# Performance work log

Hardware: AMD Instinct MI355X
Metric: run time of the kernel (lower is better)

The kernel has to match this reference:

```python
import jax, jax.numpy as jnp
import numpy as np

N, E, H, R = 16384, 262144, 256, 64
INV_SQRT_3 = 1.0 / np.sqrt(3.0)
INV_SQRT_H = 1.0 / np.sqrt(float(H))
INV_SQRT_2 = 1.0 / np.sqrt(2.0)


def ssilu(t):
    # ScaledSiLU: silu(x) / 0.6
    return jax.nn.silu(t) * (1.0 / 0.6)


def layernorm(x, g, b):
    m = jnp.mean(x, axis=-1, keepdims=True)
    v = jnp.var(x, axis=-1, keepdims=True)
    return (x - m) * jax.lax.rsqrt(v + 1e-5) * g + b


def gated_equivariant_block(x, v, Wv1, Wv2, Wu1, bu1, Wu2, bu2, out_ch):
    # x: [N, Cin], v: [N, 3, Cin]
    vec1 = jnp.linalg.norm(v @ Wv1, axis=-2)          # [N, Cin]
    vec2 = v @ Wv2                                     # [N, 3, out_ch]
    h = ssilu(jnp.concatenate([x, vec1], axis=-1) @ Wu1 + bu1) @ Wu2 + bu2
    xn, vn = h[..., :out_ch], h[..., out_ch:]
    return ssilu(xn), vn[:, None, :] * vec2


def setup_inputs() -> dict:
    key = jax.random.key(0)
    ks = iter(jax.random.split(key, 48))

    def w(shape, fan_in):
        return jax.random.normal(next(ks), shape, jnp.float32) / np.sqrt(float(fan_in))

    return {
        "x": jax.random.normal(next(ks), (N, H), jnp.float32),
        "vec": jax.random.normal(next(ks), (N, 3, H), jnp.float32),
        "edge_rbf": jax.random.uniform(next(ks), (E, R), jnp.float32),
        "edge_vector": jax.random.normal(next(ks), (E, 3), jnp.float32),
        # PaiNNMessage params
        "ln_g": jnp.ones((H,), jnp.float32), "ln_b": jnp.zeros((H,), jnp.float32),
        "W_x1": w((H, H), H), "b_x1": jnp.zeros((H,), jnp.float32),
        "W_x2": w((H, 3 * H), H), "b_x2": jnp.zeros((3 * H,), jnp.float32),
        "W_rbf": w((R, 3 * H), R), "b_rbf": jnp.zeros((3 * H,), jnp.float32),
        # PaiNNUpdate params
        "W_vp": w((H, 2 * H), H),
        "W_xv1": w((2 * H, H), 2 * H), "b_xv1": jnp.zeros((H,), jnp.float32),
        "W_xv2": w((H, 3 * H), H), "b_xv2": jnp.zeros((3 * H,), jnp.float32),
        # PaiNNOutput block 1 (H -> H//2)
        "o1_Wv1": w((H, H), H), "o1_Wv2": w((H, H // 2), H),
        "o1_Wu1": w((2 * H, H), 2 * H), "o1_bu1": jnp.zeros((H,), jnp.float32),
        "o1_Wu2": w((H, H), H), "o1_bu2": jnp.zeros((H,), jnp.float32),
        # PaiNNOutput block 2 (H//2 -> 1)
        "o2_Wv1": w((H // 2, H // 2), H // 2), "o2_Wv2": w((H // 2, 1), H // 2),
        "o2_Wu1": w((H, H // 2), H), "o2_bu1": jnp.zeros((H // 2,), jnp.float32),
        "o2_Wu2": w((H // 2, 2), H // 2), "o2_bu2": jnp.zeros((2,), jnp.float32),
        "edge_index": jax.random.randint(next(ks), (2, E), 0, N),
    }


def reference(x, vec, edge_rbf, edge_vector,
              ln_g, ln_b, W_x1, b_x1, W_x2, b_x2, W_rbf, b_rbf,
              W_vp, W_xv1, b_xv1, W_xv2, b_xv2,
              o1_Wv1, o1_Wv2, o1_Wu1, o1_bu1, o1_Wu2, o1_bu2,
              o2_Wv1, o2_Wv2, o2_Wu1, o2_bu1, o2_Wu2, o2_bu2,
              edge_index):
    src, dst = edge_index[0], edge_index[1]

    # ---- PaiNNMessage ----
    xh = ssilu(layernorm(x, ln_g, ln_b) @ W_x1 + b_x1) @ W_x2 + b_x2   # [N, 3H]
    rbfh = edge_rbf @ W_rbf + b_rbf                                     # [E, 3H]
    m = xh[src] * rbfh                                                  # gather + fuse
    m1, m2, m3 = m[:, :H], m[:, H:2 * H], m[:, 2 * H:]
    m2 = m2 * INV_SQRT_3
    vmsg = (vec[src] * m2[:, None, :] + m3[:, None, :] * edge_vector[:, :, None]) * INV_SQRT_H  # [E,3,H]
    dx = jax.ops.segment_sum(m1, dst, num_segments=N)
    dvec = jax.ops.segment_sum(vmsg, dst, num_segments=N)
    x = x + dx
    vec = vec + dvec

    # ---- PaiNNUpdate ----
    vp = vec @ W_vp                                    # [N, 3, 2H]
    vec1, vec2 = vp[..., :H], vp[..., H:]
    vec_dot = jnp.sum(vec1 * vec2, axis=1) * INV_SQRT_H            # [N, H]
    vnorm = jnp.sqrt(jnp.sum(vec2 * vec2, axis=-2) + 1e-8)          # [N, H]
    xvh = ssilu(jnp.concatenate([x, vnorm], axis=-1) @ W_xv1 + b_xv1) @ W_xv2 + b_xv2
    xv1, xv2, xv3 = xvh[:, :H], xvh[:, H:2 * H], xvh[:, 2 * H:]
    x = x + (xv1 + xv2 * vec_dot) * INV_SQRT_2
    vec = vec + xv3[:, None, :] * vec1

    # ---- PaiNNOutput ----
    x, vec = gated_equivariant_block(x, vec, o1_Wv1, o1_Wv2, o1_Wu1, o1_bu1, o1_Wu2, o1_bu2, H // 2)
    x, vec = gated_equivariant_block(x, vec, o2_Wv1, o2_Wv2, o2_Wu1, o2_bu1, o2_Wu2, o2_bu2, 1)
    return jnp.squeeze(vec, axis=-1)   # [N, 3]
```

## Files before the change

kernel.cpp:

```cpp
#include <hip/hip_runtime.h>
#include <math.h>

#define NN 16384
#define EE 262144
#define HH 256

#define INV_SQRT_3f 0.57735026918962576f
#define INV_SQRT_Hf 0.0625f
#define INV_SQRT_2f 0.70710678118654752f
#define SSILU_SCALE 1.6666666666666667f

typedef __attribute__((ext_vector_type(8))) short bf16x8;
typedef __attribute__((ext_vector_type(4))) float f32x4;

__device__ __forceinline__ float ssilu_f(float v) {
    return v * (1.0f / (1.0f + __expf(-v))) * SSILU_SCALE;
}
__device__ __forceinline__ float b2f(short s) {
    unsigned int u = ((unsigned int)(unsigned short)s) << 16;
    return __uint_as_float(u);
}
__device__ __forceinline__ short f2b(float f) {
    unsigned int u = __float_as_uint(f);
    unsigned int r = (u + 0x7fff + ((u >> 16) & 1)) >> 16;
    return (short)r;
}

__global__ void __launch_bounds__(256) ln_kernel(const float* __restrict__ x,
                                                 const float* __restrict__ g,
                                                 const float* __restrict__ b,
                                                 short* __restrict__ oh,
                                                 short* __restrict__ ol) {
    int n = blockIdx.x;
    int t = threadIdx.x;
    float v = x[(long)n * HH + t];
    float s = v, s2 = v * v;
    #pragma unroll
    for (int off = 32; off > 0; off >>= 1) {
        s  += __shfl_down(s, off);
        s2 += __shfl_down(s2, off);
    }
    __shared__ float red[8];
    int wave = t >> 6, lane = t & 63;
    if (lane == 0) { red[wave] = s; red[4 + wave] = s2; }
    __syncthreads();
    __shared__ float mr[2];
    if (t == 0) {
        float ts = red[0] + red[1] + red[2] + red[3];
        float ts2 = red[4] + red[5] + red[6] + red[7];
        float mean = ts * (1.0f / HH);
        float var = ts2 * (1.0f / HH) - mean * mean;
        mr[0] = mean;
        mr[1] = rsqrtf(var + 1e-5f);
    }
    __syncthreads();
    float o = (v - mr[0]) * mr[1] * g[t] + b[t];
    short hh = f2b(o);
    oh[(long)n * HH + t] = hh;
    ol[(long)n * HH + t] = f2b(o - b2f(hh));
}

struct WtArgs {
    const float* W[11];
    int K[11];
    int N[11];
    int off[12];
};

__global__ void __launch_bounds__(256) wt_split_all(WtArgs a,
                                                    short* __restrict__ WTh,
                                                    short* __restrict__ WTl) {
    int idx = blockIdx.x * 256 + threadIdx.x;
    int s = 0;
    #pragma unroll
    for (int i = 1; i < 11; i++) s += (idx >= a.off[i]) ? 1 : 0;
    int local = idx - a.off[s];
    int K = a.K[s], N = a.N[s];
    int k = local / N, n = local - k * N;
    float w = a.W[s][local];
    short hh = f2b(w);
    long o = (long)a.off[s] + (long)n * K + k;
    WTh[o] = hh;
    WTl[o] = f2b(w - b2f(hh));
}

__global__ void __launch_bounds__(256) split4_kernel(const float* __restrict__ in,
                                                     short* __restrict__ h,
                                                     short* __restrict__ l) {
    long i = ((long)blockIdx.x * 256 + threadIdx.x) * 4;
    float4 v = *(const float4*)(in + i);
    short4 oh, ol;
    oh.x = f2b(v.x); ol.x = f2b(v.x - b2f(oh.x));
    oh.y = f2b(v.y); ol.y = f2b(v.y - b2f(oh.y));
    oh.z = f2b(v.z); ol.z = f2b(v.z - b2f(oh.z));
    oh.w = f2b(v.w); ol.w = f2b(v.w - b2f(oh.w));
    *(short4*)(h + i) = oh;
    *(short4*)(l + i) = ol;
}

__global__ void __launch_bounds__(256) mfma_gemm(const short* __restrict__ Ah,
                                                 const short* __restrict__ Al,
                                                 const short* __restrict__ Wh,
                                                 const short* __restrict__ Wl,
                                                 const float* __restrict__ bias,
                                                 void* __restrict__ Ch,
                                                 short* __restrict__ Cl,
                                                 int M, int K, int N, int act) {
    int tid = threadIdx.x;
    int wave = tid >> 6, lane = tid & 63;
    int quad = lane >> 4, l16 = lane & 15;
    long bm = (long)blockIdx.x * 128 + wave * 32;
    long bn = (long)blockIdx.y * 64;
    long a0 = (bm + l16) * K + quad * 8;
    long a1 = a0 + (long)16 * K;
    long w0 = (bn + l16) * K + quad * 8;

    f32x4 acc[2][4];
    #pragma unroll
    for (int f = 0; f < 2; f++)
        #pragma unroll
        for (int t = 0; t < 4; t++) acc[f][t] = (f32x4){0.f, 0.f, 0.f, 0.f};

    bf16x8 cah[2], cal[2], cbh[4], cbl[4];
    cah[0] = *(const bf16x8*)(Ah + a0);
    cah[1] = *(const bf16x8*)(Ah + a1);
    cal[0] = *(const bf16x8*)(Al + a0);
    cal[1] = *(const bf16x8*)(Al + a1);
    #pragma unroll
    for (int t = 0; t < 4; t++) {
        long wo = w0 + (long)t * 16 * K;
        cbh[t] = *(const bf16x8*)(Wh + wo);
        cbl[t] = *(const bf16x8*)(Wl + wo);
    }

    for (int k0 = 0; k0 < K; k0 += 32) {
        int k1 = k0 + 32;
        bf16x8 nah[2], nal[2], nbh[4], nbl[4];
        if (k1 < K) {
            nah[0] = *(const bf16x8*)(Ah + a0 + k1);
            nah[1] = *(const bf16x8*)(Ah + a1 + k1);
            nal[0] = *(const bf16x8*)(Al + a0 + k1);
            nal[1] = *(const bf16x8*)(Al + a1 + k1);
            #pragma unroll
            for (int t = 0; t < 4; t++) {
                long wo = w0 + (long)t * 16 * K + k1;
                nbh[t] = *(const bf16x8*)(Wh + wo);
                nbl[t] = *(const bf16x8*)(Wl + wo);
            }
        }
        #pragma unroll
        for (int t = 0; t < 4; t++) {
            #pragma unroll
            for (int f = 0; f < 2; f++) {
                acc[f][t] = __builtin_amdgcn_mfma_f32_16x16x32_bf16(cah[f], cbh[t], acc[f][t], 0, 0, 0);
                acc[f][t] = __builtin_amdgcn_mfma_f32_16x16x32_bf16(cal[f], cbh[t], acc[f][t], 0, 0, 0);
                acc[f][t] = __builtin_amdgcn_mfma_f32_16x16x32_bf16(cah[f], cbl[t], acc[f][t], 0, 0, 0);
            }
        }
        if (k1 < K) {
            cah[0] = nah[0]; cah[1] = nah[1];
            cal[0] = nal[0]; cal[1] = nal[1];
            #pragma unroll
            for (int t = 0; t < 4; t++) { cbh[t] = nbh[t]; cbl[t] = nbl[t]; }
        }
    }

    #pragma unroll
    for (int f = 0; f < 2; f++) {
        long row0 = bm + f * 16 + quad * 4;
        #pragma unroll
        for (int t = 0; t < 4; t++) {
            long col = bn + t * 16 + l16;
            float bv = bias ? bias[col] : 0.f;
            #pragma unroll
            for (int r = 0; r < 4; r++) {
                float v = acc[f][t][r] + bv;
                if (act & 1) v = ssilu_f(v);
                long idx = (row0 + r) * N + col;
                if (Cl) {
                    short hh = f2b(v);
                    ((short*)Ch)[idx] = hh;
                    Cl[idx] = f2b(v - b2f(hh));
                } else if (act & 2) {
                    ((short*)Ch)[idx] = f2b(v);
                } else {
                    ((float*)Ch)[idx] = v;
                }
            }
        }
    }
}

__global__ void __launch_bounds__(256) zero_kernel(int* __restrict__ p, int n) {
    int i = blockIdx.x * 256 + threadIdx.x;
    if (i < n) p[i] = 0;
}

__global__ void __launch_bounds__(256) hist_kernel(const int* __restrict__ eidx,
                                                   int* __restrict__ cnt) {
    int e = blockIdx.x * 256 + threadIdx.x;
    atomicAdd(&cnt[eidx[EE + e]], 1);
}

__global__ void __launch_bounds__(256) scan_kernel(int* __restrict__ cursor,
                                                   int* __restrict__ rowptr) {
    int t = threadIdx.x;
    int base_i = t * 64;
    int tsum = 0;
    for (int i = 0; i < 64; i++) tsum += cursor[base_i + i];
    __shared__ int ls[256];
    ls[t] = tsum;
    __syncthreads();
    for (int off = 1; off < 256; off <<= 1) {
        int v = (t >= off) ? ls[t - off] : 0;
        __syncthreads();
        ls[t] += v;
        __syncthreads();
    }
    int running = ls[t] - tsum;
    for (int i = 0; i < 64; i++) {
        int c = cursor[base_i + i];
        rowptr[base_i + i] = running;
        cursor[base_i + i] = running;
        running += c;
    }
    if (t == 255) rowptr[NN] = running;
}

__global__ void __launch_bounds__(256) scatter_kernel(const int* __restrict__ eidx,
                                                      int* __restrict__ cursor,
                                                      int* __restrict__ perm) {
    int e = blockIdx.x * 256 + threadIdx.x;
    int d_ = eidx[EE + e];
    int pos = atomicAdd(&cursor[d_], 1);
    perm[pos] = e;
}

__global__ void __launch_bounds__(256) deg_hist_kernel(const int* __restrict__ rowptr,
                                                       int* __restrict__ dhist) {
    int n = blockIdx.x * 256 + threadIdx.x;
    int deg = rowptr[n + 1] - rowptr[n];
    atomicAdd(&dhist[min(deg, 63)], 1);
}

__global__ void __launch_bounds__(64) deg_scan_kernel(int* __restrict__ dhist) {
    if (threadIdx.x == 0) {
        int run = 0;
        for (int b = 63; b >= 0; b--) {
            int c = dhist[b];
            dhist[b] = run;
            run += c;
        }
    }
}

__global__ void __launch_bounds__(256) deg_scatter_kernel(const int* __restrict__ rowptr,
                                                          int* __restrict__ dhist,
                                                          int* __restrict__ nodeorder) {
    int n = blockIdx.x * 256 + threadIdx.x;
    int deg = min(rowptr[n + 1] - rowptr[n], 63);
    int pos = atomicAdd(&dhist[deg], 1);
    nodeorder[pos] = n;
}

#define EPB 16

template <int NE>
__device__ __forceinline__ void rbf_gemm(const float* __restrict__ W_rbf, int t,
                                         const float (&rbf_s)[EPB][64],
                                         float bb1, float bb2, float bb3,
                                         float* __restrict__ acc1,
                                         float* __restrict__ acc2,
                                         float* __restrict__ acc3) {
    #pragma unroll
    for (int e = 0; e < NE; e++) { acc1[e] = bb1; acc2[e] = bb2; acc3[e] = bb3; }
    for (int k = 0; k < 64; k++) {
        float w1 = W_rbf[k * 768 + t];
        float w2 = W_rbf[k * 768 + 256 + t];
        float w3 = W_rbf[k * 768 + 512 + t];
        #pragma unroll
        for (int e = 0; e < NE; e++) {
            float r = rbf_s[e][k];
            acc1[e] += r * w1;
            acc2[e] += r * w2;
            acc3[e] += r * w3;
        }
    }
}

__global__ void __launch_bounds__(256) node_gather_kernel(
        const float* __restrict__ rbf,
        const float* __restrict__ W_rbf,
        const float* __restrict__ b_rbf,
        const float* __restrict__ xh,
        const float* __restrict__ vec,
        const float* __restrict__ ev,
        const int* __restrict__ eidx,
        const float* __restrict__ x,
        const int* __restrict__ perm,
        const int* __restrict__ rowptr,
        const int* __restrict__ nodeorder,
        float* __restrict__ x1,
        float* __restrict__ vecacc,
        short* __restrict__ vah,
        short* __restrict__ val) {
    int n = nodeorder[blockIdx.x];
    int t = threadIdx.x;
    int beg = rowptr[n], deg = rowptr[n + 1] - beg;

    __shared__ float rbf_s[EPB][64];
    __shared__ int eid_s[EPB], src_s[EPB];
    __shared__ float ev_s[EPB][3];

    float bb1 = b_rbf[t], bb2 = b_rbf[256 + t], bb3 = b_rbf[512 + t];
    float dxa = 0.f, dv0 = 0.f, dv1 = 0.f, dv2 = 0.f;
    float acc1[EPB], acc2[EPB], acc3[EPB];

    for (int b0 = 0; b0 < deg; b0 += EPB) {
        int cnt = min(EPB, deg - b0);
        __syncthreads();
        if (t < cnt) {
            int eid = perm[beg + b0 + t];
            eid_s[t] = eid;
            src_s[t] = eidx[eid];
        }
        __syncthreads();
        #pragma unroll
        for (int i = 0; i < (EPB * 64) / 256; i++) {
            int idx = i * 256 + t;
            int e = idx >> 6, k = idx & 63;
            rbf_s[e][k] = (e < cnt) ? rbf[(long)eid_s[e] * 64 + k] : 0.f;
        }
        if (t < cnt * 3) {
            int e = t / 3, d = t % 3;
            ev_s[e][d] = ev[(long)eid_s[e] * 3 + d];
        }
        __syncthreads();

        if (cnt > 8)      rbf_gemm<16>(W_rbf, t, rbf_s, bb1, bb2, bb3, acc1, acc2, acc3);
        else if (cnt > 4) rbf_gemm<8>(W_rbf, t, rbf_s, bb1, bb2, bb3, acc1, acc2, acc3);
        else              rbf_gemm<4>(W_rbf, t, rbf_s, bb1, bb2, bb3, acc1, acc2, acc3);

        #define EDGE_ACC(e)                                                   \
            {                                                                 \
                int s = src_s[e];                                             \
                const float* xr = xh + (long)s * 768;                         \
                const float* vr = vec + (long)s * 768;                        \
                float m1 = acc1[e] * xr[t];                                   \
                float m2 = acc2[e] * xr[256 + t] * INV_SQRT_3f;               \
                float m3 = acc3[e] * xr[512 + t];                             \
                dxa += m1;                                                    \
                dv0 += (vr[t] * m2       + m3 * ev_s[e][0]) * INV_SQRT_Hf;    \
                dv1 += (vr[256 + t] * m2 + m3 * ev_s[e][1]) * INV_SQRT_Hf;    \
                dv2 += (vr[512 + t] * m2 + m3 * ev_s[e][2]) * INV_SQRT_Hf;    \
            }

        if (cnt == EPB) {
            #pragma unroll 4
            for (int e = 0; e < EPB; e++) EDGE_ACC(e)
        } else {
            for (int e = 0; e < cnt; e++) EDGE_ACC(e)
        }
        #undef EDGE_ACC
    }

    long nb = (long)n * 256 + t;
    x1[nb] = x[nb] + dxa;
    long vb = (long)n * 768 + t;
    float vv0 = vec[vb] + dv0;
    float vv1 = vec[vb + 256] + dv1;
    float vv2 = vec[vb + 512] + dv2;
    vecacc[vb]       = vv0;
    vecacc[vb + 256] = vv1;
    vecacc[vb + 512] = vv2;
    short h0 = f2b(vv0), h1 = f2b(vv1), h2 = f2b(vv2);
    vah[vb]       = h0;  val[vb]       = f2b(vv0 - b2f(h0));
    vah[vb + 256] = h1;  val[vb + 256] = f2b(vv1 - b2f(h1));
    vah[vb + 512] = h2;  val[vb + 512] = f2b(vv2 - b2f(h2));
}

__global__ void __launch_bounds__(256) vdot_cat_kernel(const float* __restrict__ vec1,
                                                       const short* __restrict__ vec2,
                                                       const float* __restrict__ x1,
                                                       float* __restrict__ vdot,
                                                       short* __restrict__ cath,
                                                       short* __restrict__ catl) {
    int idx = blockIdx.x * 256 + threadIdx.x;
    int n = idx >> 8, h = idx & 255;
    float dsum = 0.f, s2 = 0.f;
    #pragma unroll
    for (int d = 0; d < 3; d++) {
        long r = (long)(n * 3 + d) * 256 + h;
        float a = vec1[r];
        float b = b2f(vec2[r]);
        dsum += a * b;
        s2 += b * b;
    }
    vdot[idx] = dsum * INV_SQRT_Hf;
    float xv = x1[idx];
    short hh = f2b(xv);
    cath[(long)n * 512 + h] = hh;
    catl[(long)n * 512 + h] = f2b(xv - b2f(hh));
    float vn = sqrtf(s2 + 1e-8f);
    short vh = f2b(vn);
    cath[(long)n * 512 + 256 + h] = vh;
    catl[(long)n * 512 + 256 + h] = f2b(vn - b2f(vh));
}

__global__ void __launch_bounds__(256) e4_kernel(float* __restrict__ x1,
                                                 float* __restrict__ vecacc,
                                                 const float* __restrict__ vec1,
                                                 const float* __restrict__ vdot,
                                                 const short* __restrict__ xvh_h,
                                                 const short* __restrict__ xvh_l) {
    int idx = blockIdx.x * 256 + threadIdx.x;
    int n = idx >> 8, h = idx & 255;
    long b0 = (long)n * 768 + h;
    float xv1 = b2f(xvh_h[b0])       + b2f(xvh_l[b0]);
    float xv2 = b2f(xvh_h[b0 + 256]) + b2f(xvh_l[b0 + 256]);
    float xv3 = b2f(xvh_h[b0 + 512]) + b2f(xvh_l[b0 + 512]);
    x1[idx] = x1[idx] + (xv1 + xv2 * vdot[idx]) * INV_SQRT_2f;
    #pragma unroll
    for (int d = 0; d < 3; d++) {
        long r = (long)(n * 3 + d) * 256 + h;
        vecacc[r] = vecacc[r] + xv3 * vec1[r];
    }
}

__global__ void __launch_bounds__(256) normcat_kernel(const float* __restrict__ xin,
                                                      const short* __restrict__ w,
                                                      short* __restrict__ cath,
                                                      short* __restrict__ catl,
                                                      int Cx, int C, int shift) {
    int idx = blockIdx.x * 256 + threadIdx.x;
    int cols = 1 << shift;
    int n = idx >> shift, c = idx & (cols - 1);
    float v;
    if (c < Cx) {
        v = xin[(long)n * Cx + c];
    } else {
        int cc = c - Cx;
        float s = 0.f;
        #pragma unroll
        for (int d = 0; d < 3; d++) {
            float a = b2f(w[(long)(n * 3 + d) * C + cc]);
            s += a * a;
        }
        v = sqrtf(s);
    }
    short hh = f2b(v);
    cath[idx] = hh;
    catl[idx] = f2b(v - b2f(hh));
}

__global__ void __launch_bounds__(256) gate1_kernel(const float* __restrict__ h1,
                                                    const short* __restrict__ w2h,
                                                    const short* __restrict__ w2l,
                                                    float* __restrict__ x3,
                                                    short* __restrict__ vecCh,
                                                    short* __restrict__ vecCl) {
    int idx = blockIdx.x * 256 + threadIdx.x;
    int n = idx >> 7, c = idx & 127;
    x3[idx] = ssilu_f(h1[(long)n * 256 + c]);
    float vn = h1[(long)n * 256 + 128 + c];
    #pragma unroll
    for (int d = 0; d < 3; d++) {
        long r = (long)(n * 3 + d) * 128 + c;
        float wv = b2f(w2h[r]) + b2f(w2l[r]);
        float v = vn * wv;
        short hh = f2b(v);
        vecCh[r] = hh;
        vecCl[r] = f2b(v - b2f(hh));
    }
}

__global__ void __launch_bounds__(256) g12_kernel(const short* __restrict__ vecCh,
                                                  const short* __restrict__ vecCl,
                                                  const float* __restrict__ Wv2,
                                                  float* __restrict__ w4) {
    int row = blockIdx.x * 4 + (threadIdx.x >> 6);
    int lane = threadIdx.x & 63;
    long r0 = (long)row * 128 + lane;
    float v0 = b2f(vecCh[r0]) + b2f(vecCl[r0]);
    float v1 = b2f(vecCh[r0 + 64]) + b2f(vecCl[r0 + 64]);
    float s = v0 * Wv2[lane] + v1 * Wv2[64 + lane];
    #pragma unroll
    for (int off = 32; off > 0; off >>= 1) s += __shfl_down(s, off);
    if (lane == 0) w4[row] = s;
}

__global__ void __launch_bounds__(256) final_kernel(const float* __restrict__ t5,
                                                    const float* __restrict__ Wu2,
                                                    const float* __restrict__ bu2,
                                                    const float* __restrict__ w4,
                                                    float* __restrict__ out) {
    int n = blockIdx.x * 4 + (threadIdx.x >> 6);
    int lane = threadIdx.x & 63;
    float s = t5[(long)n * 128 + lane] * Wu2[lane * 2 + 1] +
              t5[(long)n * 128 + 64 + lane] * Wu2[(64 + lane) * 2 + 1];
    #pragma unroll
    for (int off = 32; off > 0; off >>= 1) s += __shfl_down(s, off);
    float val = __shfl(s, 0) + bu2[1];
    if (lane < 3) out[(long)n * 3 + lane] = val * w4[(long)n * 3 + lane];
}

extern "C" void kernel_launch(void* const* d_in, const int* in_sizes, int n_in,
                              void* d_out, int out_size, void* d_ws, size_t ws_size,
                              hipStream_t stream) {
    const float* x          = (const float*)d_in[0];
    const float* vec        = (const float*)d_in[1];
    const float* edge_rbf   = (const float*)d_in[2];
    const float* edge_vector= (const float*)d_in[3];
    const float* ln_g       = (const float*)d_in[4];
    const float* ln_b       = (const float*)d_in[5];
    const float* W_x1       = (const float*)d_in[6];
    const float* b_x1       = (const float*)d_in[7];
    const float* W_x2       = (const float*)d_in[8];
    const float* b_x2       = (const float*)d_in[9];
    const float* W_rbf      = (const float*)d_in[10];
    const float* b_rbf      = (const float*)d_in[11];
    const float* W_vp       = (const float*)d_in[12];
    const float* W_xv1      = (const float*)d_in[13];
    const float* b_xv1      = (const float*)d_in[14];
    const float* W_xv2      = (const float*)d_in[15];
    const float* b_xv2      = (const float*)d_in[16];
    const float* o1_Wv1     = (const float*)d_in[17];
    const float* o1_Wv2     = (const float*)d_in[18];
    const float* o1_Wu1     = (const float*)d_in[19];
    const float* o1_bu1     = (const float*)d_in[20];
    const float* o1_Wu2     = (const float*)d_in[21];
    const float* o1_bu2     = (const float*)d_in[22];
    const float* o2_Wv1     = (const float*)d_in[23];
    const float* o2_Wv2     = (const float*)d_in[24];
    const float* o2_Wu1     = (const float*)d_in[25];
    const float* o2_bu1     = (const float*)d_in[26];
    const float* o2_Wu2     = (const float*)d_in[27];
    const float* o2_bu2     = (const float*)d_in[28];
    const int*   edge_index = (const int*)d_in[29];
    float* out = (float*)d_out;
    float* ws  = (float*)d_ws;

    const size_t S = (size_t)NN * 256;
    const size_t Q = S / 4;
    float* x1      = ws;
    float* vecacc  = ws + 4 * Q;
    short* wtb     = (short*)(ws + 16 * Q);
    const long WLO = 1064960;
    short* xln_h = (short*)(ws + 18 * Q);
    short* xln_l = (short*)(ws + 20 * Q);
    short* t1_h  = (short*)(ws + 22 * Q);
    short* t1_l  = (short*)(ws + 24 * Q);
    float* xh    = ws + 30 * Q;
    int* rowptr    = (int*)(ws + 48 * Q);
    int* cursor    = rowptr + (NN + 1);
    int* dhist     = cursor + NN;
    int* nodeorder = dhist + 64;
    int* perm      = nodeorder + NN;
    short* vah   = (short*)(ws + 18 * Q);
    short* val_  = (short*)(ws + 24 * Q);
    float* vec1  = ws + 30 * Q;
    short* vec2b = (short*)(ws + 42 * Q);
    float* vdot  = ws + 48 * Q;
    short* catb_h = (short*)(ws + 18 * Q);
    short* catb_l = (short*)(ws + 22 * Q);
    short* t2_h  = (short*)(ws + 26 * Q);
    short* t2_l  = (short*)(ws + 28 * Q);
    short* xvh_h = (short*)(ws + 18 * Q);
    short* xvh_l = (short*)(ws + 42 * Q);
    short* vah2  = (short*)(ws + 18 * Q);
    short* val2  = (short*)(ws + 24 * Q);
    short* w1b   = (short*)(ws + 30 * Q);
    short* w2_h  = (short*)(ws + 36 * Q);
    short* w2_l  = (short*)(ws + 39 * Q);
    short* cat2_h = (short*)(ws + 42 * Q);
    short* cat2_l = (short*)(ws + 46 * Q);
    short* t4_h  = (short*)(ws + 18 * Q);
    short* t4_l  = (short*)(ws + 20 * Q);
    float* h1    = ws + 22 * Q;
    float* x3    = ws + 26 * Q;
    short* vecC_h = (short*)(ws + 28 * Q);
    short* vecC_l = (short*)(ws + 31 * Q);
    short* w3b   = (short*)(ws + 34 * Q);
    float* w4    = ws + 37 * Q;
    short* cat3_h = (short*)(ws + 38 * Q);
    short* cat3_l = (short*)(ws + 40 * Q);
    float* t5    = ws + 42 * Q;

    short* WT_x1    = wtb;
    short* WT_x2    = wtb + 65536;
    short* WT_vp    = wtb + 262144;
    short* WT_xv1   = wtb + 393216;
    short* WT_xv2   = wtb + 524288;
    short* WT_o1Wv1 = wtb + 720896;
    short* WT_o1Wv2 = wtb + 786432;
    short* WT_o1Wu1 = wtb + 819200;
    short* WT_o1Wu2 = wtb + 950272;
    short* WT_o2Wv1 = wtb + 1015808;
    short* WT_o2Wu1 = wtb + 1032192;

    WtArgs wa;
    const float* wsrc[11] = {W_x1, W_x2, W_vp, W_xv1, W_xv2, o1_Wv1, o1_Wv2,
                             o1_Wu1, o1_Wu2, o2_Wv1, o2_Wu1};
    int wk[11] = {256, 256, 256, 512, 256, 256, 256, 512, 256, 128, 256};
    int wn[11] = {256, 768, 512, 256, 768, 256, 128, 256, 256, 128, 128};
    int off = 0;
    for (int i = 0; i < 11; i++) {
        wa.W[i] = wsrc[i]; wa.K[i] = wk[i]; wa.N[i] = wn[i];
        wa.off[i] = off; off += wk[i] * wn[i];
    }
    wa.off[11] = off;
    wt_split_all<<<off / 256, 256, 0, stream>>>(wa, wtb, wtb + WLO);

    ln_kernel<<<NN, 256, 0, stream>>>(x, ln_g, ln_b, xln_h, xln_l);
    mfma_gemm<<<dim3(NN / 128, 4), 256, 0, stream>>>(xln_h, xln_l, WT_x1, WT_x1 + WLO,
                                                     b_x1, t1_h, t1_l, NN, 256, 256, 1);
    mfma_gemm<<<dim3(NN / 128, 12), 256, 0, stream>>>(t1_h, t1_l, WT_x2, WT_x2 + WLO,
                                                      b_x2, xh, nullptr, NN, 256, 768, 0);

    zero_kernel<<<(NN + 64 + 255) / 256, 256, 0, stream>>>(cursor, NN + 64);
    hist_kernel<<<EE / 256, 256, 0, stream>>>(edge_index, cursor);
    scan_kernel<<<1, 256, 0, stream>>>(cursor, rowptr);
    scatter_kernel<<<EE / 256, 256, 0, stream>>>(edge_index, cursor, perm);
    deg_hist_kernel<<<NN / 256, 256, 0, stream>>>(rowptr, dhist);
    deg_scan_kernel<<<1, 64, 0, stream>>>(dhist);
    deg_scatter_kernel<<<NN / 256, 256, 0, stream>>>(rowptr, dhist, nodeorder);
    node_gather_kernel<<<NN, 256, 0, stream>>>(edge_rbf, W_rbf, b_rbf, xh, vec,
                                               edge_vector, edge_index, x,
                                               perm, rowptr, nodeorder, x1, vecacc,
                                               vah, val_);

    mfma_gemm<<<dim3(3 * NN / 128, 4), 256, 0, stream>>>(vah, val_, WT_vp, WT_vp + WLO,
                                                         nullptr, vec1, nullptr,
                                                         3 * NN, 256, 256, 0);
    mfma_gemm<<<dim3(3 * NN / 128, 4), 256, 0, stream>>>(vah, val_, WT_vp + 65536,
                                                         WT_vp + WLO + 65536,
                                                         nullptr, vec2b, nullptr,
                                                         3 * NN, 256, 256, 2);
    vdot_cat_kernel<<<NN, 256, 0, stream>>>(vec1, vec2b, x1, vdot, catb_h, catb_l);
    mfma_gemm<<<dim3(NN / 128, 4), 256, 0, stream>>>(catb_h, catb_l, WT_xv1, WT_xv1 + WLO,
                                                     b_xv1, t2_h, t2_l, NN, 512, 256, 1);
    mfma_gemm<<<dim3(NN / 128, 12), 256, 0, stream>>>(t2_h, t2_l, WT_xv2, WT_xv2 + WLO,
                                                      b_xv2, xvh_h, xvh_l, NN, 256, 768, 0);
    e4_kernel<<<NN, 256, 0, stream>>>(x1, vecacc, vec1, vdot, xvh_h, xvh_l);

    split4_kernel<<<3 * S / 1024, 256, 0, stream>>>(vecacc, vah2, val2);
    mfma_gemm<<<dim3(3 * NN / 128, 4), 256, 0, stream>>>(vah2, val2, WT_o1Wv1, WT_o1Wv1 + WLO,
                                                         nullptr, w1b, nullptr,
                                                         3 * NN, 256, 256, 2);
    mfma_gemm<<<dim3(3 * NN / 128, 2), 256, 0, stream>>>(vah2, val2, WT_o1Wv2, WT_o1Wv2 + WLO,
                                                         nullptr, w2_h, w2_l,
                                                         3 * NN, 256, 128, 0);
    normcat_kernel<<<NN * 512 / 256, 256, 0, stream>>>(x1, w1b, cat2_h, cat2_l, 256, 256, 9);
    mfma_gemm<<<dim3(NN / 128, 4), 256, 0, stream>>>(cat2_h, cat2_l, WT_o1Wu1, WT_o1Wu1 + WLO,
                                                     o1_bu1, t4_h, t4_l, NN, 512, 256, 1);
    mfma_gemm<<<dim3(NN / 128, 4), 256, 0, stream>>>(t4_h, t4_l, WT_o1Wu2, WT_o1Wu2 + WLO,
                                                     o1_bu2, h1, nullptr, NN, 256, 256, 0);
    gate1_kernel<<<NN * 128 / 256, 256, 0, stream>>>(h1, w2_h, w2_l, x3, vecC_h, vecC_l);

    mfma_gemm<<<dim3(3 * NN / 128, 2), 256, 0, stream>>>(vecC_h, vecC_l, WT_o2Wv1,
                                                         WT_o2Wv1 + WLO, nullptr,
                                                         w3b, nullptr, 3 * NN, 128, 128, 2);
    g12_kernel<<<3 * NN / 4, 256, 0, stream>>>(vecC_h, vecC_l, o2_Wv2, w4);
    normcat_kernel<<<NN * 256 / 256, 256, 0, stream>>>(x3, w3b, cat3_h, cat3_l, 128, 128, 8);
    mfma_gemm<<<dim3(NN / 128, 2), 256, 0, stream>>>(cat3_h, cat3_l, WT_o2Wu1, WT_o2Wu1 + WLO,
                                                     o2_bu1, t5, nullptr, NN, 256, 128, 1);
    final_kernel<<<NN / 4, 256, 0, stream>>>(t5, o2_Wu2, o2_bu2, w4, out);
}
```

Before: 1.681 ms.

## Compute per-edge RBF projection with split-bf16 MFMA and fuse bf16 split into e4

```diff
diff --git a/kernel.cpp b/kernel.cpp
--- a/kernel.cpp
+++ b/kernel.cpp
@@ -61,10 +61,10 @@
 }
 
 struct WtArgs {
-    const float* W[11];
-    int K[11];
-    int N[11];
-    int off[12];
+    const float* W[12];
+    int K[12];
+    int N[12];
+    int off[13];
 };
 
 __global__ void __launch_bounds__(256) wt_split_all(WtArgs a,
@@ -73,7 +73,7 @@
     int idx = blockIdx.x * 256 + threadIdx.x;
     int s = 0;
     #pragma unroll
-    for (int i = 1; i < 11; i++) s += (idx >= a.off[i]) ? 1 : 0;
+    for (int i = 1; i < 12; i++) s += (idx >= a.off[i]) ? 1 : 0;
     int local = idx - a.off[s];
     int K = a.K[s], N = a.N[s];
     int k = local / N, n = local - k * N;
@@ -82,20 +82,6 @@
     long o = (long)a.off[s] + (long)n * K + k;
     WTh[o] = hh;
     WTl[o] = f2b(w - b2f(hh));
-}
-
-__global__ void __launch_bounds__(256) split4_kernel(const float* __restrict__ in,
-                                                     short* __restrict__ h,
-                                                     short* __restrict__ l) {
-    long i = ((long)blockIdx.x * 256 + threadIdx.x) * 4;
-    float4 v = *(const float4*)(in + i);
-    short4 oh, ol;
-    oh.x = f2b(v.x); ol.x = f2b(v.x - b2f(oh.x));
-    oh.y = f2b(v.y); ol.y = f2b(v.y - b2f(oh.y));
-    oh.z = f2b(v.z); ol.z = f2b(v.z - b2f(oh.z));
-    oh.w = f2b(v.w); ol.w = f2b(v.w - b2f(oh.w));
-    *(short4*)(h + i) = oh;
-    *(short4*)(l + i) = ol;
 }
 
 __global__ void __launch_bounds__(256) mfma_gemm(const short* __restrict__ Ah,
@@ -264,33 +250,10 @@
 }
 
 #define EPB 16
-
-template <int NE>
-__device__ __forceinline__ void rbf_gemm(const float* __restrict__ W_rbf, int t,
-                                         const float (&rbf_s)[EPB][64],
-                                         float bb1, float bb2, float bb3,
-                                         float* __restrict__ acc1,
-                                         float* __restrict__ acc2,
-                                         float* __restrict__ acc3) {
-    #pragma unroll
-    for (int e = 0; e < NE; e++) { acc1[e] = bb1; acc2[e] = bb2; acc3[e] = bb3; }
-    for (int k = 0; k < 64; k++) {
-        float w1 = W_rbf[k * 768 + t];
-        float w2 = W_rbf[k * 768 + 256 + t];
-        float w3 = W_rbf[k * 768 + 512 + t];
-        #pragma unroll
-        for (int e = 0; e < NE; e++) {
-            float r = rbf_s[e][k];
-            acc1[e] += r * w1;
-            acc2[e] += r * w2;
-            acc3[e] += r * w3;
-        }
-    }
-}
-
 __global__ void __launch_bounds__(256) node_gather_kernel(
         const float* __restrict__ rbf,
-        const float* __restrict__ W_rbf,
+        const short* __restrict__ WTr_h,
+        const short* __restrict__ WTr_l,
         const float* __restrict__ b_rbf,
         const float* __restrict__ xh,
         const float* __restrict__ vec,
@@ -306,21 +269,32 @@
         short* __restrict__ val) {
     int n = nodeorder[blockIdx.x];
     int t = threadIdx.x;
+    int wave = t >> 6, lane = t & 63;
+    int quad = lane >> 4, l16 = lane & 15;
     int beg = rowptr[n], deg = rowptr[n + 1] - beg;
 
-    __shared__ float rbf_s[EPB][64];
+    __shared__ short a_h[EPB][72];
+    __shared__ short a_l[EPB][72];
     __shared__ int eid_s[EPB], src_s[EPB];
     __shared__ float ev_s[EPB][3];
 
-    float bb1 = b_rbf[t], bb2 = b_rbf[256 + t], bb3 = b_rbf[512 + t];
-    float dxa = 0.f, dv0 = 0.f, dv1 = 0.f, dv2 = 0.f;
-    float acc1[EPB], acc2[EPB], acc3[EPB];
+    float bb[3][4];
+    #pragma unroll
+    for (int g = 0; g < 3; g++)
+        #pragma unroll
+        for (int tt = 0; tt < 4; tt++)
+            bb[g][tt] = b_rbf[g * 256 + wave * 64 + tt * 16 + l16];
+
+    float dxa[4] = {0.f, 0.f, 0.f, 0.f};
+    float dv0[4] = {0.f, 0.f, 0.f, 0.f};
+    float dv1[4] = {0.f, 0.f, 0.f, 0.f};
+    float dv2[4] = {0.f, 0.f, 0.f, 0.f};
 
     for (int b0 = 0; b0 < deg; b0 += EPB) {
         int cnt = min(EPB, deg - b0);
         __syncthreads();
-        if (t < cnt) {
-            int eid = perm[beg + b0 + t];
+        if (t < EPB) {
+            int eid = perm[beg + b0 + ((t < cnt) ? t : 0)];
             eid_s[t] = eid;
             src_s[t] = eidx[eid];
         }
@@ -329,7 +303,10 @@
         for (int i = 0; i < (EPB * 64) / 256; i++) {
             int idx = i * 256 + t;
             int e = idx >> 6, k = idx & 63;
-            rbf_s[e][k] = (e < cnt) ? rbf[(long)eid_s[e] * 64 + k] : 0.f;
+            float r = (e < cnt) ? rbf[(long)eid_s[e] * 64 + k] : 0.f;
+            short hh = f2b(r);
+            a_h[e][k] = hh;
+            a_l[e][k] = f2b(r - b2f(hh));
         }
         if (t < cnt * 3) {
             int e = t / 3, d = t % 3;
@@ -337,46 +314,80 @@
         }
         __syncthreads();
 
-        if (cnt > 8)      rbf_gemm<16>(W_rbf, t, rbf_s, bb1, bb2, bb3, acc1, acc2, acc3);
-        else if (cnt > 4) rbf_gemm<8>(W_rbf, t, rbf_s, bb1, bb2, bb3, acc1, acc2, acc3);
-        else              rbf_gemm<4>(W_rbf, t, rbf_s, bb1, bb2, bb3, acc1, acc2, acc3);
-
-        #define EDGE_ACC(e)                                                   \
-            {                                                                 \
-                int s = src_s[e];                                             \
-                const float* xr = xh + (long)s * 768;                         \
-                const float* vr = vec + (long)s * 768;                        \
-                float m1 = acc1[e] * xr[t];                                   \
-                float m2 = acc2[e] * xr[256 + t] * INV_SQRT_3f;               \
-                float m3 = acc3[e] * xr[512 + t];                             \
-                dxa += m1;                                                    \
-                dv0 += (vr[t] * m2       + m3 * ev_s[e][0]) * INV_SQRT_Hf;    \
-                dv1 += (vr[256 + t] * m2 + m3 * ev_s[e][1]) * INV_SQRT_Hf;    \
-                dv2 += (vr[512 + t] * m2 + m3 * ev_s[e][2]) * INV_SQRT_Hf;    \
+        f32x4 acc[3][4];
+        #pragma unroll
+        for (int g = 0; g < 3; g++)
+            #pragma unroll
+            for (int tt = 0; tt < 4; tt++) acc[g][tt] = (f32x4){0.f, 0.f, 0.f, 0.f};
+        #pragma unroll
+        for (int kc = 0; kc < 2; kc++) {
+            bf16x8 ah = *(const bf16x8*)(&a_h[l16][kc * 32 + quad * 8]);
+            bf16x8 al = *(const bf16x8*)(&a_l[l16][kc * 32 + quad * 8]);
+            #pragma unroll
+            for (int g = 0; g < 3; g++) {
+                #pragma unroll
+                for (int tt = 0; tt < 4; tt++) {
+                    long col = g * 256 + wave * 64 + tt * 16 + l16;
+                    long wo = col * 64 + kc * 32 + quad * 8;
+                    bf16x8 bh = *(const bf16x8*)(WTr_h + wo);
+                    bf16x8 bl = *(const bf16x8*)(WTr_l + wo);
+                    acc[g][tt] = __builtin_amdgcn_mfma_f32_16x16x32_bf16(ah, bh, acc[g][tt], 0, 0, 0);
+                    acc[g][tt] = __builtin_amdgcn_mfma_f32_16x16x32_bf16(al, bh, acc[g][tt], 0, 0, 0);
+                    acc[g][tt] = __builtin_amdgcn_mfma_f32_16x16x32_bf16(ah, bl, acc[g][tt], 0, 0, 0);
+                }
             }
-
-        if (cnt == EPB) {
-            #pragma unroll 4
-            for (int e = 0; e < EPB; e++) EDGE_ACC(e)
-        } else {
-            for (int e = 0; e < cnt; e++) EDGE_ACC(e)
-        }
-        #undef EDGE_ACC
-    }
-
-    long nb = (long)n * 256 + t;
-    x1[nb] = x[nb] + dxa;
-    long vb = (long)n * 768 + t;
-    float vv0 = vec[vb] + dv0;
-    float vv1 = vec[vb + 256] + dv1;
-    float vv2 = vec[vb + 512] + dv2;
-    vecacc[vb]       = vv0;
-    vecacc[vb + 256] = vv1;
-    vecacc[vb + 512] = vv2;
-    short h0 = f2b(vv0), h1 = f2b(vv1), h2 = f2b(vv2);
-    vah[vb]       = h0;  val[vb]       = f2b(vv0 - b2f(h0));
-    vah[vb + 256] = h1;  val[vb + 256] = f2b(vv1 - b2f(h1));
-    vah[vb + 512] = h2;  val[vb + 512] = f2b(vv2 - b2f(h2));
+        }
+
+        #pragma unroll
+        for (int r = 0; r < 4; r++) {
+            int e = quad * 4 + r;
+            bool valid = (e < cnt);
+            int s = src_s[e];
+            const float* xr = xh + (long)s * 768;
+            const float* vr = vec + (long)s * 768;
+            float e0 = ev_s[e][0], e1 = ev_s[e][1], e2 = ev_s[e][2];
+            #pragma unroll
+            for (int tt = 0; tt < 4; tt++) {
+                int c = wave * 64 + tt * 16 + l16;
+                float m1 = (acc[0][tt][r] + bb[0][tt]) * xr[c];
+                float m2 = (acc[1][tt][r] + bb[1][tt]) * xr[256 + c] * INV_SQRT_3f;
+                float m3 = (acc[2][tt][r] + bb[2][tt]) * xr[512 + c];
+                if (valid) {
+                    dxa[tt] += m1;
+                    dv0[tt] += (vr[c] * m2       + m3 * e0) * INV_SQRT_Hf;
+                    dv1[tt] += (vr[256 + c] * m2 + m3 * e1) * INV_SQRT_Hf;
+                    dv2[tt] += (vr[512 + c] * m2 + m3 * e2) * INV_SQRT_Hf;
+                }
+            }
+        }
+    }
+
+    #pragma unroll
+    for (int tt = 0; tt < 4; tt++) {
+        dxa[tt] += __shfl_xor(dxa[tt], 16); dxa[tt] += __shfl_xor(dxa[tt], 32);
+        dv0[tt] += __shfl_xor(dv0[tt], 16); dv0[tt] += __shfl_xor(dv0[tt], 32);
+        dv1[tt] += __shfl_xor(dv1[tt], 16); dv1[tt] += __shfl_xor(dv1[tt], 32);
+        dv2[tt] += __shfl_xor(dv2[tt], 16); dv2[tt] += __shfl_xor(dv2[tt], 32);
+    }
+    if (quad == 0) {
+        #pragma unroll
+        for (int tt = 0; tt < 4; tt++) {
+            int c = wave * 64 + tt * 16 + l16;
+            long nb = (long)n * 256 + c;
+            x1[nb] = x[nb] + dxa[tt];
+            long vb = (long)n * 768 + c;
+            float vv0 = vec[vb]       + dv0[tt];
+            float vv1 = vec[vb + 256] + dv1[tt];
+            float vv2 = vec[vb + 512] + dv2[tt];
+            vecacc[vb]       = vv0;
+            vecacc[vb + 256] = vv1;
+            vecacc[vb + 512] = vv2;
+            short h0 = f2b(vv0), h1 = f2b(vv1), h2 = f2b(vv2);
+            vah[vb]       = h0;  val[vb]       = f2b(vv0 - b2f(h0));
+            vah[vb + 256] = h1;  val[vb + 256] = f2b(vv1 - b2f(h1));
+            vah[vb + 512] = h2;  val[vb + 512] = f2b(vv2 - b2f(h2));
+        }
+    }
 }
 
 __global__ void __launch_bounds__(256) vdot_cat_kernel(const float* __restrict__ vec1,
@@ -412,7 +423,9 @@
                                                  const float* __restrict__ vec1,
                                                  const float* __restrict__ vdot,
                                                  const short* __restrict__ xvh_h,
-                                                 const short* __restrict__ xvh_l) {
+                                                 const short* __restrict__ xvh_l,
+                                                 short* __restrict__ vah2,
+                                                 short* __restrict__ val2) {
     int idx = blockIdx.x * 256 + threadIdx.x;
     int n = idx >> 8, h = idx & 255;
     long b0 = (long)n * 768 + h;
@@ -423,7 +436,11 @@
     #pragma unroll
     for (int d = 0; d < 3; d++) {
         long r = (long)(n * 3 + d) * 256 + h;
-        vecacc[r] = vecacc[r] + xv3 * vec1[r];
+        float vv = vecacc[r] + xv3 * vec1[r];
+        vecacc[r] = vv;
+        short hh = f2b(vv);
+        vah2[r] = hh;
+        val2[r] = f2b(vv - b2f(hh));
     }
 }
 
@@ -545,7 +562,7 @@
     float* x1      = ws;
     float* vecacc  = ws + 4 * Q;
     short* wtb     = (short*)(ws + 16 * Q);
-    const long WLO = 1064960;
+    const long WLO = 1114112;
     short* xln_h = (short*)(ws + 18 * Q);
     short* xln_l = (short*)(ws + 20 * Q);
     short* t1_h  = (short*)(ws + 22 * Q);
@@ -597,18 +614,19 @@
     short* WT_o1Wu2 = wtb + 950272;
     short* WT_o2Wv1 = wtb + 1015808;
     short* WT_o2Wu1 = wtb + 1032192;
+    short* WT_rbf   = wtb + 1064960;
 
     WtArgs wa;
-    const float* wsrc[11] = {W_x1, W_x2, W_vp, W_xv1, W_xv2, o1_Wv1, o1_Wv2,
-                             o1_Wu1, o1_Wu2, o2_Wv1, o2_Wu1};
-    int wk[11] = {256, 256, 256, 512, 256, 256, 256, 512, 256, 128, 256};
-    int wn[11] = {256, 768, 512, 256, 768, 256, 128, 256, 256, 128, 128};
+    const float* wsrc[12] = {W_x1, W_x2, W_vp, W_xv1, W_xv2, o1_Wv1, o1_Wv2,
+                             o1_Wu1, o1_Wu2, o2_Wv1, o2_Wu1, W_rbf};
+    int wk[12] = {256, 256, 256, 512, 256, 256, 256, 512, 256, 128, 256, 64};
+    int wn[12] = {256, 768, 512, 256, 768, 256, 128, 256, 256, 128, 128, 768};
     int off = 0;
-    for (int i = 0; i < 11; i++) {
+    for (int i = 0; i < 12; i++) {
         wa.W[i] = wsrc[i]; wa.K[i] = wk[i]; wa.N[i] = wn[i];
         wa.off[i] = off; off += wk[i] * wn[i];
     }
-    wa.off[11] = off;
+    wa.off[12] = off;
     wt_split_all<<<off / 256, 256, 0, stream>>>(wa, wtb, wtb + WLO);
 
     ln_kernel<<<NN, 256, 0, stream>>>(x, ln_g, ln_b, xln_h, xln_l);
@@ -624,8 +642,8 @@
     deg_hist_kernel<<<NN / 256, 256, 0, stream>>>(rowptr, dhist);
     deg_scan_kernel<<<1, 64, 0, stream>>>(dhist);
     deg_scatter_kernel<<<NN / 256, 256, 0, stream>>>(rowptr, dhist, nodeorder);
-    node_gather_kernel<<<NN, 256, 0, stream>>>(edge_rbf, W_rbf, b_rbf, xh, vec,
-                                               edge_vector, edge_index, x,
+    node_gather_kernel<<<NN, 256, 0, stream>>>(edge_rbf, WT_rbf, WT_rbf + WLO, b_rbf,
+                                               xh, vec, edge_vector, edge_index, x,
                                                perm, rowptr, nodeorder, x1, vecacc,
                                                vah, val_);
 
@@ -641,9 +659,8 @@
                                                      b_xv1, t2_h, t2_l, NN, 512, 256, 1);
     mfma_gemm<<<dim3(NN / 128, 12), 256, 0, stream>>>(t2_h, t2_l, WT_xv2, WT_xv2 + WLO,
                                                       b_xv2, xvh_h, xvh_l, NN, 256, 768, 0);
-    e4_kernel<<<NN, 256, 0, stream>>>(x1, vecacc, vec1, vdot, xvh_h, xvh_l);
-
-    split4_kernel<<<3 * S / 1024, 256, 0, stream>>>(vecacc, vah2, val2);
+    e4_kernel<<<NN, 256, 0, stream>>>(x1, vecacc, vec1, vdot, xvh_h, xvh_l, vah2, val2);
+
     mfma_gemm<<<dim3(3 * NN / 128, 4), 256, 0, stream>>>(vah2, val2, WT_o1Wv1, WT_o1Wv1 + WLO,
                                                          nullptr, w1b, nullptr,
                                                          3 * NN, 256, 256, 2);
```

Measured after the change: 2.457 ms. 1.46x slower.
